# Performance work log

Measured on AMD Instinct MI355X. Metric: run time of the kernel, lower is better.

## Reference

```python
import jax, jax.numpy as jnp
import numpy as np

N_NODES = 50000
N_EDGES = 800000
D = 128
NEG_SLOPE = 0.01
LN_EPS = 1e-5


def gcn_conv(x, W, b, src, dst, n_nodes):
    # Linear transform: [N, D_in] @ [D_in, D_out]
    h = x @ W
    # Symmetric degree normalization (self-loops already included in src/dst)
    deg = jax.ops.segment_sum(jnp.ones_like(dst, dtype=h.dtype), dst, num_segments=n_nodes)
    dinv = jnp.where(deg > 0, jax.lax.rsqrt(deg), 0.0)
    coef = dinv[src] * dinv[dst]                      # [E]
    msg = h[src] * coef[:, None]                      # gather + scale, [E, D]
    out = jax.ops.segment_sum(msg, dst, num_segments=n_nodes)  # scatter-add
    return out + b


def layer_norm(x, gamma, beta):
    mu = jnp.mean(x, axis=-1, keepdims=True)
    var = jnp.mean(jnp.square(x - mu), axis=-1, keepdims=True)
    return (x - mu) * jax.lax.rsqrt(var + LN_EPS) * gamma + beta


def setup_inputs() -> dict:
    key = jax.random.key(0)
    ks = jax.random.split(key, 8)
    x = jax.random.normal(ks[0], (N_NODES, D), dtype=jnp.float32)
    edge_index = jax.random.randint(ks[1], (2, N_EDGES), 0, N_NODES, dtype=jnp.int64)
    s = 1.0 / np.sqrt(D)
    W1 = jax.random.uniform(ks[2], (D, D), jnp.float32, -s, s)
    b1 = jnp.zeros((D,), jnp.float32)
    W2 = jax.random.uniform(ks[3], (D, D), jnp.float32, -s, s)
    b2 = jnp.zeros((D,), jnp.float32)
    ln1_g = jnp.ones((D,), jnp.float32)
    ln1_b = jnp.zeros((D,), jnp.float32)
    ln2_g = jnp.ones((D,), jnp.float32)
    ln2_b = jnp.zeros((D,), jnp.float32)
    return {"x": x, "edge_index": edge_index, "W1": W1, "b1": b1,
            "ln1_g": ln1_g, "ln1_b": ln1_b, "W2": W2, "b2": b2,
            "ln2_g": ln2_g, "ln2_b": ln2_b}


def reference(x, edge_index, W1, b1, ln1_g, ln1_b, W2, b2, ln2_g, ln2_b):
    n = x.shape[0]
    # add self-loops (PyG GCNConv default)
    loops = jnp.arange(n, dtype=edge_index.dtype)
    src = jnp.concatenate([edge_index[0], loops])
    dst = jnp.concatenate([edge_index[1], loops])

    residual = x
    h = gcn_conv(x, W1, b1, src, dst, n)
    h = jax.nn.leaky_relu(h, NEG_SLOPE)
    h = layer_norm(h + residual, ln1_g, ln1_b)
    h = gcn_conv(h, W2, b2, src, dst, n)
    return jax.nn.leaky_relu(layer_norm(h + residual, ln2_g, ln2_b), NEG_SLOPE)
```

## Files before the change

### kernel.cpp

```cpp
#include <hip/hip_runtime.h>
#include <hip/hip_bf16.h>

#define NN 50000
#define NE 800000
#define D 128
#define NEG_SLOPE 0.01f
#define LN_EPS 1e-5f

#define NPB 256
#define NB 196
#define CAP 6144
#define ECH 8192
#define NCH ((NE + ECH - 1) / ECH)
#define NWPK 128

typedef __attribute__((ext_vector_type(8))) short bf16x8;
typedef __attribute__((ext_vector_type(4))) float f32x4;
typedef __attribute__((ext_vector_type(4))) int i32x4;

__device__ inline unsigned short f2bf(float f) {
    unsigned u = __float_as_uint(f);
    unsigned r = 0x7FFFu + ((u >> 16) & 1u);
    return (unsigned short)((u + r) >> 16);
}
__device__ inline void bf2x(unsigned u, float& lo, float& hi) {
    lo = __uint_as_float(u << 16);
    hi = __uint_as_float(u & 0xFFFF0000u);
}

__global__ __launch_bounds__(256) void fused_a(const int* __restrict__ src,
                                               const int* __restrict__ dst,
                                               int* __restrict__ bcursor,
                                               unsigned* __restrict__ bedge,
                                               const float* __restrict__ W1,
                                               const float* __restrict__ W2,
                                               unsigned short* __restrict__ WT1,
                                               unsigned short* __restrict__ WT2,
                                               unsigned short* __restrict__ hbf,
                                               unsigned short* __restrict__ hbf2) {
    __shared__ int hist[NB], lcur[NB], gbase[NB];
    int bid = blockIdx.x, t = threadIdx.x;
    if (bid < NCH) {
        int e0 = bid * ECH;
        int ecnt = min(ECH, NE - e0);
        if (t < NB) hist[t] = 0;
        __syncthreads();
        for (int k = t; k < ecnt; k += 256) atomicAdd(&hist[dst[e0 + k] >> 8], 1);
        __syncthreads();
        if (t < NB) {
            gbase[t] = atomicAdd(&bcursor[t], hist[t]);
            lcur[t] = 0;
        }
        __syncthreads();
        for (int k = t; k < ecnt; k += 256) {
            int s = src[e0 + k], d = dst[e0 + k];
            int b = d >> 8;
            int p = atomicAdd(&lcur[b], 1);
            bedge[(size_t)b * CAP + gbase[b] + p] = (unsigned)s | ((unsigned)(d & 255) << 16);
        }
    } else {
        int tid = (bid - NCH) * 256 + t;
        if (tid < 32) {
            uint4 z = make_uint4(0u, 0u, 0u, 0u);
            if (tid < 16) *(uint4*)&hbf[(size_t)NN * D + tid * 8] = z;
            else          *(uint4*)&hbf2[(size_t)NN * D + (tid - 16) * 8] = z;
        }
        const float* W = (tid < D * D) ? W1 : W2;
        unsigned short* WT = (tid < D * D) ? WT1 : WT2;
        int id = tid & (D * D - 1);
        int nn = id & 127, k = id >> 7;
        WT[nn * 128 + k] = f2bf(W[k * 128 + nn]);
    }
}

__global__ __launch_bounds__(256) void fused_b(const unsigned* __restrict__ bedge,
                                               const int* __restrict__ bcnt,
                                               float* __restrict__ dinv,
                                               int2* __restrict__ rowinfo,
                                               int* __restrict__ ticket,
                                               int* __restrict__ csr_src) {
    __shared__ int h[NPB];
    __shared__ int tmp[256];
    __shared__ int rl[NPB], cur[NPB];
    __shared__ int base;
    int b = blockIdx.x, t = threadIdx.x;
    h[t] = 0;
    __syncthreads();
    int s0 = b * CAP, s1 = s0 + bcnt[b];
    for (int k = s0 + t; k < s1; k += 256) atomicAdd(&h[bedge[k] >> 16], 1);
    __syncthreads();
    int deg = h[t];
    int node = b * NPB + t;
    int pdeg = (deg + 7) & ~7;
    tmp[t] = pdeg;
    __syncthreads();
    for (int off = 1; off < 256; off <<= 1) {
        int uu = (t >= off) ? tmp[t - off] : 0;
        __syncthreads();
        tmp[t] += uu;
        __syncthreads();
    }
    if (t == 255) base = atomicAdd(ticket, tmp[255]);
    __syncthreads();
    int start = base + tmp[t] - pdeg;
    rl[t] = start;
    cur[t] = 0;
    if (node < NN) {
        dinv[node] = rsqrtf((float)(deg + 1));
        rowinfo[node] = make_int2(start, pdeg);
    }
    __syncthreads();
    for (int k = s0 + t; k < s1; k += 256) {
        unsigned w = bedge[k];
        int li = w >> 16;
        int p = atomicAdd(&cur[li], 1);
        csr_src[rl[li] + p] = (int)(w & 0xFFFFu);
    }
    __syncthreads();
    int dgc = cur[t];
    int pend = (dgc + 7) & ~7;
    for (int k = dgc; k < pend; ++k)
        csr_src[rl[t] + k] = NN;
}

__global__ __launch_bounds__(256) void gemm_mfma(const float* __restrict__ A,
                                                 const unsigned short* __restrict__ WT,
                                                 const float* __restrict__ dinv,
                                                 unsigned short* __restrict__ out, int n) {
    __shared__ __align__(16) unsigned short a_lds[64 * 128];
    __shared__ __align__(16) unsigned short w_lds[128 * 128];
    int t = threadIdx.x;
    int m0 = blockIdx.x * 64;

    #pragma unroll
    for (int it = 0; it < 8; ++it) {
        int idx = it * 256 + t;
        int row = idx >> 4, c = idx & 15;
        uint4 v = *(const uint4*)&WT[row * 128 + c * 8];
        int byte = (row * 256 + c * 16) ^ ((row & 7) << 4);
        *(uint4*)((char*)w_lds + byte) = v;
    }
    #pragma unroll
    for (int it = 0; it < 4; ++it) {
        int idx = it * 256 + t;
        int row = idx >> 4, c = idx & 15;
        int grow = m0 + row;
        uint4 w = make_uint4(0u, 0u, 0u, 0u);
        if (grow < n) {
            float4 v0 = *(const float4*)&A[(size_t)grow * D + c * 8];
            float4 v1 = *(const float4*)&A[(size_t)grow * D + c * 8 + 4];
            w.x = (unsigned)f2bf(v0.x) | ((unsigned)f2bf(v0.y) << 16);
            w.y = (unsigned)f2bf(v0.z) | ((unsigned)f2bf(v0.w) << 16);
            w.z = (unsigned)f2bf(v1.x) | ((unsigned)f2bf(v1.y) << 16);
            w.w = (unsigned)f2bf(v1.z) | ((unsigned)f2bf(v1.w) << 16);
        }
        int byte = (row * 256 + c * 16) ^ ((row & 7) << 4);
        *(uint4*)((char*)a_lds + byte) = w;
    }
    __syncthreads();

    int wv = t >> 6, l = t & 63;
    int lrow = l & 15, lgrp = l >> 4;
    int arow = wv * 16 + lrow;

    f32x4 acc[8];
    #pragma unroll
    for (int nf = 0; nf < 8; ++nf) acc[nf] = (f32x4){0.f, 0.f, 0.f, 0.f};

    #pragma unroll
    for (int kk = 0; kk < 4; ++kk) {
        int abyte = (arow * 256 + kk * 64 + lgrp * 16) ^ ((arow & 7) << 4);
        bf16x8 afrag = *(bf16x8*)((char*)a_lds + abyte);
        #pragma unroll
        for (int nf = 0; nf < 8; ++nf) {
            int bcol = nf * 16 + lrow;
            int bbyte = (bcol * 256 + kk * 64 + lgrp * 16) ^ ((bcol & 7) << 4);
            bf16x8 bfrag = *(bf16x8*)((char*)w_lds + bbyte);
            acc[nf] = __builtin_amdgcn_mfma_f32_16x16x32_bf16(afrag, bfrag, acc[nf], 0, 0, 0);
        }
    }

    #pragma unroll
    for (int r = 0; r < 4; ++r) {
        int grow = m0 + wv * 16 + lgrp * 4 + r;
        if (grow < n) {
            float dv = dinv[grow];
            #pragma unroll
            for (int nf = 0; nf < 8; ++nf)
                out[(size_t)grow * D + nf * 16 + lrow] = f2bf(dv * acc[nf][r]);
        }
    }
}


__device__ inline void agg8s(const unsigned* __restrict__ h, const int* __restrict__ csr,
                             int e, int lane, float& ax_, float& ay_) {
    i32x4 s0 = __builtin_nontemporal_load((const i32x4*)(csr + e));
    i32x4 s1 = __builtin_nontemporal_load((const i32x4*)(csr + e + 4));
    unsigned g0 = h[(size_t)s0[0] * (D / 2) + lane];
    unsigned g1 = h[(size_t)s0[1] * (D / 2) + lane];
    unsigned g2 = h[(size_t)s0[2] * (D / 2) + lane];
    unsigned g3 = h[(size_t)s0[3] * (D / 2) + lane];
    unsigned g4 = h[(size_t)s1[0] * (D / 2) + lane];
    unsigned g5 = h[(size_t)s1[1] * (D / 2) + lane];
    unsigned g6 = h[(size_t)s1[2] * (D / 2) + lane];
    unsigned g7 = h[(size_t)s1[3] * (D / 2) + lane];
    float lo, hi;
    bf2x(g0, lo, hi); ax_ += lo; ay_ += hi;
    bf2x(g1, lo, hi); ax_ += lo; ay_ += hi;
    bf2x(g2, lo, hi); ax_ += lo; ay_ += hi;
    bf2x(g3, lo, hi); ax_ += lo; ay_ += hi;
    bf2x(g4, lo, hi); ax_ += lo; ay_ += hi;
    bf2x(g5, lo, hi); ax_ += lo; ay_ += hi;
    bf2x(g6, lo, hi); ax_ += lo; ay_ += hi;
    bf2x(g7, lo, hi); ax_ += lo; ay_ += hi;
}

__device__ inline void agg_2node(const unsigned* __restrict__ h,
                                 const int* __restrict__ csr,
                                 int eA, int eA1, int eB, int eB1, int lane,
                                 float& aAx, float& aAy, float& aBx, float& aBy) {
    while (eA + 16 <= eA1 && eB + 16 <= eB1) {
        i32x4 sA0 = __builtin_nontemporal_load((const i32x4*)(csr + eA));
        i32x4 sA1 = __builtin_nontemporal_load((const i32x4*)(csr + eA + 4));
        i32x4 sA2 = __builtin_nontemporal_load((const i32x4*)(csr + eA + 8));
        i32x4 sA3 = __builtin_nontemporal_load((const i32x4*)(csr + eA + 12));
        i32x4 sB0 = __builtin_nontemporal_load((const i32x4*)(csr + eB));
        i32x4 sB1 = __builtin_nontemporal_load((const i32x4*)(csr + eB + 4));
        i32x4 sB2 = __builtin_nontemporal_load((const i32x4*)(csr + eB + 8));
        i32x4 sB3 = __builtin_nontemporal_load((const i32x4*)(csr + eB + 12));
        unsigned gA0 = h[(size_t)sA0[0] * (D / 2) + lane];
        unsigned gA1 = h[(size_t)sA0[1] * (D / 2) + lane];
        unsigned gA2 = h[(size_t)sA0[2] * (D / 2) + lane];
        unsigned gA3 = h[(size_t)sA0[3] * (D / 2) + lane];
        unsigned gA4 = h[(size_t)sA1[0] * (D / 2) + lane];
        unsigned gA5 = h[(size_t)sA1[1] * (D / 2) + lane];
        unsigned gA6 = h[(size_t)sA1[2] * (D / 2) + lane];
        unsigned gA7 = h[(size_t)sA1[3] * (D / 2) + lane];
        unsigned gA8 = h[(size_t)sA2[0] * (D / 2) + lane];
        unsigned gA9 = h[(size_t)sA2[1] * (D / 2) + lane];
        unsigned gAa = h[(size_t)sA2[2] * (D / 2) + lane];
        unsigned gAb = h[(size_t)sA2[3] * (D / 2) + lane];
        unsigned gAc = h[(size_t)sA3[0] * (D / 2) + lane];
        unsigned gAd = h[(size_t)sA3[1] * (D / 2) + lane];
        unsigned gAe = h[(size_t)sA3[2] * (D / 2) + lane];
        unsigned gAf = h[(size_t)sA3[3] * (D / 2) + lane];
        unsigned gB0 = h[(size_t)sB0[0] * (D / 2) + lane];
        unsigned gB1 = h[(size_t)sB0[1] * (D / 2) + lane];
        unsigned gB2 = h[(size_t)sB0[2] * (D / 2) + lane];
        unsigned gB3 = h[(size_t)sB0[3] * (D / 2) + lane];
        unsigned gB4 = h[(size_t)sB1[0] * (D / 2) + lane];
        unsigned gB5 = h[(size_t)sB1[1] * (D / 2) + lane];
        unsigned gB6 = h[(size_t)sB1[2] * (D / 2) + lane];
        unsigned gB7 = h[(size_t)sB1[3] * (D / 2) + lane];
        unsigned gB8 = h[(size_t)sB2[0] * (D / 2) + lane];
        unsigned gB9 = h[(size_t)sB2[1] * (D / 2) + lane];
        unsigned gBa = h[(size_t)sB2[2] * (D / 2) + lane];
        unsigned gBb = h[(size_t)sB2[3] * (D / 2) + lane];
        unsigned gBc = h[(size_t)sB3[0] * (D / 2) + lane];
        unsigned gBd = h[(size_t)sB3[1] * (D / 2) + lane];
        unsigned gBe = h[(size_t)sB3[2] * (D / 2) + lane];
        unsigned gBf = h[(size_t)sB3[3] * (D / 2) + lane];
        float lo, hi;
        bf2x(gA0, lo, hi); aAx += lo; aAy += hi;
        bf2x(gA1, lo, hi); aAx += lo; aAy += hi;
        bf2x(gA2, lo, hi); aAx += lo; aAy += hi;
        bf2x(gA3, lo, hi); aAx += lo; aAy += hi;
        bf2x(gA4, lo, hi); aAx += lo; aAy += hi;
        bf2x(gA5, lo, hi); aAx += lo; aAy += hi;
        bf2x(gA6, lo, hi); aAx += lo; aAy += hi;
        bf2x(gA7, lo, hi); aAx += lo; aAy += hi;
        bf2x(gA8, lo, hi); aAx += lo; aAy += hi;
        bf2x(gA9, lo, hi); aAx += lo; aAy += hi;
        bf2x(gAa, lo, hi); aAx += lo; aAy += hi;
        bf2x(gAb, lo, hi); aAx += lo; aAy += hi;
        bf2x(gAc, lo, hi); aAx += lo; aAy += hi;
        bf2x(gAd, lo, hi); aAx += lo; aAy += hi;
        bf2x(gAe, lo, hi); aAx += lo; aAy += hi;
        bf2x(gAf, lo, hi); aAx += lo; aAy += hi;
        bf2x(gB0, lo, hi); aBx += lo; aBy += hi;
        bf2x(gB1, lo, hi); aBx += lo; aBy += hi;
        bf2x(gB2, lo, hi); aBx += lo; aBy += hi;
        bf2x(gB3, lo, hi); aBx += lo; aBy += hi;
        bf2x(gB4, lo, hi); aBx += lo; aBy += hi;
        bf2x(gB5, lo, hi); aBx += lo; aBy += hi;
        bf2x(gB6, lo, hi); aBx += lo; aBy += hi;
        bf2x(gB7, lo, hi); aBx += lo; aBy += hi;
        bf2x(gB8, lo, hi); aBx += lo; aBy += hi;
        bf2x(gB9, lo, hi); aBx += lo; aBy += hi;
        bf2x(gBa, lo, hi); aBx += lo; aBy += hi;
        bf2x(gBb, lo, hi); aBx += lo; aBy += hi;
        bf2x(gBc, lo, hi); aBx += lo; aBy += hi;
        bf2x(gBd, lo, hi); aBx += lo; aBy += hi;
        bf2x(gBe, lo, hi); aBx += lo; aBy += hi;
        bf2x(gBf, lo, hi); aBx += lo; aBy += hi;
        eA += 16; eB += 16;
    }
    while (eA + 8 <= eA1 && eB + 8 <= eB1) {
        agg8s(h, csr, eA, lane, aAx, aAy);
        agg8s(h, csr, eB, lane, aBx, aBy);
        eA += 8; eB += 8;
    }
    while (eA < eA1) { agg8s(h, csr, eA, lane, aAx, aAy); eA += 8; }
    while (eB < eB1) { agg8s(h, csr, eB, lane, aBx, aBy); eB += 8; }
}

__global__ __launch_bounds__(512) void agg_ln1_gemm(const unsigned* __restrict__ h,
                                                    const float* __restrict__ x,
                                                    const float* __restrict__ bias,
                                                    const float* __restrict__ gamma,
                                                    const float* __restrict__ beta,
                                                    const float* __restrict__ dinv,
                                                    const int2* __restrict__ rowinfo,
                                                    const int* __restrict__ csr_src,
                                                    const unsigned short* __restrict__ wt2,
                                                    unsigned short* __restrict__ hbf2) {
    __shared__ __align__(16) unsigned short w_lds[128 * 128];
    __shared__ __align__(16) unsigned short a_lds[16 * 128];
    int t = threadIdx.x;

    #pragma unroll
    for (int it = 0; it < 4; ++it) {
        int idx = it * 512 + t;
        int row = idx >> 4, c = idx & 15;
        uint4 v = *(const uint4*)&wt2[row * 128 + c * 8];
        int byte = (row * 256 + c * 16) ^ ((row & 7) << 4);
        *(uint4*)((char*)w_lds + byte) = v;
    }

    int wid = t >> 6, lane = t & 63;
    int iA = blockIdx.x * 16 + wid * 2;
    int iB = iA + 1;
    float diA = dinv[iA], diB = dinv[iB];

    float aAx, aAy, aBx, aBy;
    bf2x(h[(size_t)iA * (D / 2) + lane], aAx, aAy);
    bf2x(h[(size_t)iB * (D / 2) + lane], aBx, aBy);

    int2 riA = rowinfo[iA];
    int2 riB = rowinfo[iB];
    int eA = __builtin_amdgcn_readfirstlane(riA.x);
    int eA1 = eA + __builtin_amdgcn_readfirstlane(riA.y);
    int eB = __builtin_amdgcn_readfirstlane(riB.x);
    int eB1 = eB + __builtin_amdgcn_readfirstlane(riB.y);
    agg_2node(h, csr_src, eA, eA1, eB, eB1, lane, aAx, aAy, aBx, aBy);

    float2 bv = *(const float2*)&bias[2 * lane];
    float2 gv = *(const float2*)&gamma[2 * lane];
    float2 bt = *(const float2*)&beta[2 * lane];

    aAx = fmaf(diA, aAx, bv.x); aAy = fmaf(diA, aAy, bv.y);
    aBx = fmaf(diB, aBx, bv.x); aBy = fmaf(diB, aBy, bv.y);
    aAx = aAx > 0.f ? aAx : NEG_SLOPE * aAx;
    aAy = aAy > 0.f ? aAy : NEG_SLOPE * aAy;
    aBx = aBx > 0.f ? aBx : NEG_SLOPE * aBx;
    aBy = aBy > 0.f ? aBy : NEG_SLOPE * aBy;

    size_t rowA = (size_t)iA * D + 2 * lane;
    size_t rowB = (size_t)iB * D + 2 * lane;
    float2 xA = *(const float2*)&x[rowA];
    float2 xB = *(const float2*)&x[rowB];
    float vA0 = aAx + xA.x, vA1 = aAy + xA.y;
    float vB0 = aBx + xB.x, vB1 = aBy + xB.y;

    float sA1 = vA0 + vA1, sA2 = vA0 * vA0 + vA1 * vA1;
    float sB1 = vB0 + vB1, sB2 = vB0 * vB0 + vB1 * vB1;
    #pragma unroll
    for (int off = 1; off < 64; off <<= 1) {
        sA1 += __shfl_xor(sA1, off, 64);
        sA2 += __shfl_xor(sA2, off, 64);
        sB1 += __shfl_xor(sB1, off, 64);
        sB2 += __shfl_xor(sB2, off, 64);
    }
    float muA = sA1 * (1.f / 128.f);
    float varA = fmaxf(sA2 * (1.f / 128.f) - muA * muA, 0.f);
    float rsA = rsqrtf(varA + LN_EPS);
    float muB = sB1 * (1.f / 128.f);
    float varB = fmaxf(sB2 * (1.f / 128.f) - muB * muB, 0.f);
    float rsB = rsqrtf(varB + LN_EPS);

    float oA0 = (vA0 - muA) * rsA * gv.x + bt.x;
    float oA1 = (vA1 - muA) * rsA * gv.y + bt.y;
    float oB0 = (vB0 - muB) * rsB * gv.x + bt.x;
    float oB1 = (vB1 - muB) * rsB * gv.y + bt.y;

    int rA = wid * 2, rB = wid * 2 + 1;
    unsigned dwA = (unsigned)f2bf(oA0) | ((unsigned)f2bf(oA1) << 16);
    unsigned dwB = (unsigned)f2bf(oB0) | ((unsigned)f2bf(oB1) << 16);
    int byteA = (rA * 256 + lane * 4) ^ ((rA & 7) << 4);
    int byteB = (rB * 256 + lane * 4) ^ ((rB & 7) << 4);
    *(unsigned*)((char*)a_lds + byteA) = dwA;
    *(unsigned*)((char*)a_lds + byteB) = dwB;
    __syncthreads();

    int lrow = lane & 15, lgrp = lane >> 4;
    f32x4 acc = (f32x4){0.f, 0.f, 0.f, 0.f};
    #pragma unroll
    for (int kk = 0; kk < 4; ++kk) {
        int abyte = (lrow * 256 + kk * 64 + lgrp * 16) ^ ((lrow & 7) << 4);
        bf16x8 afrag = *(bf16x8*)((char*)a_lds + abyte);
        int bcol = wid * 16 + lrow;
        int bbyte = (bcol * 256 + kk * 64 + lgrp * 16) ^ ((bcol & 7) << 4);
        bf16x8 bfrag = *(bf16x8*)((char*)w_lds + bbyte);
        acc = __builtin_amdgcn_mfma_f32_16x16x32_bf16(afrag, bfrag, acc, 0, 0, 0);
    }
    #pragma unroll
    for (int r = 0; r < 4; ++r) {
        int grow = blockIdx.x * 16 + lgrp * 4 + r;
        hbf2[(size_t)grow * D + wid * 16 + lrow] = f2bf(dinv[grow] * acc[r]);
    }
}

__global__ __launch_bounds__(256) void agg_ln2(const unsigned* __restrict__ h,
                                               const float* __restrict__ x,
                                               const float* __restrict__ bias,
                                               const float* __restrict__ gamma,
                                               const float* __restrict__ beta,
                                               const float* __restrict__ dinv,
                                               const int2* __restrict__ rowinfo,
                                               const int* __restrict__ csr_src,
                                               float* __restrict__ out) {
    int wid = threadIdx.x >> 6;
    int lane = threadIdx.x & 63;
    int iA = blockIdx.x * 8 + wid * 2;
    int iB = iA + 1;
    float diA = dinv[iA], diB = dinv[iB];

    float aAx, aAy, aBx, aBy;
    bf2x(h[(size_t)iA * (D / 2) + lane], aAx, aAy);
    bf2x(h[(size_t)iB * (D / 2) + lane], aBx, aBy);

    int2 riA = rowinfo[iA];
    int2 riB = rowinfo[iB];
    int eA = __builtin_amdgcn_readfirstlane(riA.x);
    int eA1 = eA + __builtin_amdgcn_readfirstlane(riA.y);
    int eB = __builtin_amdgcn_readfirstlane(riB.x);
    int eB1 = eB + __builtin_amdgcn_readfirstlane(riB.y);
    agg_2node(h, csr_src, eA, eA1, eB, eB1, lane, aAx, aAy, aBx, aBy);

    float2 bv = *(const float2*)&bias[2 * lane];
    float2 gv = *(const float2*)&gamma[2 * lane];
    float2 bt = *(const float2*)&beta[2 * lane];

    aAx = fmaf(diA, aAx, bv.x); aAy = fmaf(diA, aAy, bv.y);
    aBx = fmaf(diB, aBx, bv.x); aBy = fmaf(diB, aBy, bv.y);
    size_t rowA = (size_t)iA * D + 2 * lane;
    size_t rowB = (size_t)iB * D + 2 * lane;
    float2 xA = *(const float2*)&x[rowA];
    float2 xB = *(const float2*)&x[rowB];
    float vA0 = aAx + xA.x, vA1 = aAy + xA.y;
    float vB0 = aBx + xB.x, vB1 = aBy + xB.y;

    float sA1 = vA0 + vA1, sA2 = vA0 * vA0 + vA1 * vA1;
    float sB1 = vB0 + vB1, sB2 = vB0 * vB0 + vB1 * vB1;
    #pragma unroll
    for (int off = 1; off < 64; off <<= 1) {
        sA1 += __shfl_xor(sA1, off, 64);
        sA2 += __shfl_xor(sA2, off, 64);
        sB1 += __shfl_xor(sB1, off, 64);
        sB2 += __shfl_xor(sB2, off, 64);
    }
    float muA = sA1 * (1.f / 128.f);
    float varA = fmaxf(sA2 * (1.f / 128.f) - muA * muA, 0.f);
    float rsA = rsqrtf(varA + LN_EPS);
    float muB = sB1 * (1.f / 128.f);
    float varB = fmaxf(sB2 * (1.f / 128.f) - muB * muB, 0.f);
    float rsB = rsqrtf(varB + LN_EPS);

    float oA0 = (vA0 - muA) * rsA * gv.x + bt.x;
    float oA1 = (vA1 - muA) * rsA * gv.y + bt.y;
    float oB0 = (vB0 - muB) * rsB * gv.x + bt.x;
    float oB1 = (vB1 - muB) * rsB * gv.y + bt.y;
    oA0 = oA0 > 0.f ? oA0 : NEG_SLOPE * oA0;
    oA1 = oA1 > 0.f ? oA1 : NEG_SLOPE * oA1;
    oB0 = oB0 > 0.f ? oB0 : NEG_SLOPE * oB0;
    oB1 = oB1 > 0.f ? oB1 : NEG_SLOPE * oB1;
    *(float2*)&out[rowA] = make_float2(oA0, oA1);
    *(float2*)&out[rowB] = make_float2(oB0, oB1);
}

extern "C" void kernel_launch(void* const* d_in, const int* in_sizes, int n_in,
                              void* d_out, int out_size, void* d_ws, size_t ws_size,
                              hipStream_t stream) {
    const float* x    = (const float*)d_in[0];
    const int*   ei   = (const int*)d_in[1];
    const float* W1   = (const float*)d_in[2];
    const float* b1   = (const float*)d_in[3];
    const float* ln1g = (const float*)d_in[4];
    const float* ln1b = (const float*)d_in[5];
    const float* W2   = (const float*)d_in[6];
    const float* b2   = (const float*)d_in[7];
    const float* ln2g = (const float*)d_in[8];
    const float* ln2b = (const float*)d_in[9];
    float* out = (float*)d_out;

    const int* srcp = ei;
    const int* dstp = ei + NE;

    char* ws = (char*)d_ws;
    size_t p = 0;
    auto alloc = [&](size_t bytes) {
        char* r = ws + p;
        p += (bytes + 255) & ~(size_t)255;
        return r;
    };
    int*      bcursor  = (int*)alloc((NB + 1) * 4);
    int2*     rowinfo  = (int2*)alloc((size_t)NN * 8);
    float*    dinv     = (float*)alloc(NN * 4);
    unsigned* bedge    = (unsigned*)alloc((size_t)NB * CAP * 4);
    int*      csr_src  = (int*)alloc(((size_t)NE + 8 * NN) * 4);
    unsigned short* hbf  = (unsigned short*)alloc((size_t)(NN + 8) * D * 2);
    unsigned short* hbf2 = (unsigned short*)alloc((size_t)(NN + 8) * D * 2);
    unsigned short* wt1  = (unsigned short*)alloc(D * D * 2);
    unsigned short* wt2  = (unsigned short*)alloc(D * D * 2);

    hipMemsetAsync(bcursor, 0, (NB + 1) * 4, stream);

    fused_a<<<NCH + NWPK, 256, 0, stream>>>(srcp, dstp, bcursor, bedge,
                                            W1, W2, wt1, wt2, hbf, hbf2);

    fused_b<<<NB, 256, 0, stream>>>(bedge, bcursor, dinv, rowinfo,
                                    &bcursor[NB], csr_src);

    gemm_mfma<<<(NN + 63) / 64, 256, 0, stream>>>(x, wt1, dinv, hbf, NN);

    agg_ln1_gemm<<<NN / 16, 512, 0, stream>>>((const unsigned*)hbf, x, b1, ln1g, ln1b,
                                              dinv, rowinfo, csr_src, wt2, hbf2);

    agg_ln2<<<NN / 8, 256, 0, stream>>>((const unsigned*)hbf2, x, b2, ln2g, ln2b,
                                        dinv, rowinfo, csr_src, out);
}
```

Baseline: 126.2 us.

## Compute degrees via global atomics and co-launch CSR fill with first GEMM

Degree counting moves into fused_a as extra blocks doing global atomic increments per edge. A tiny dinv_rowinfo kernel then builds dinv and row offsets. The CSR fill blocks and the first MFMA GEMM blocks are merged into one launch sharing LDS through a union, so the GEMM no longer waits behind the CSR construction. This trades a separate launch and serialization for 800k extra global atomics and one more small kernel.

```diff
diff --git a/kernel.cpp b/kernel.cpp
--- a/kernel.cpp
+++ b/kernel.cpp
@@ -12,7 +12,9 @@
 #define CAP 6144
 #define ECH 8192
 #define NCH ((NE + ECH - 1) / ECH)
+#define NDEG 256
 #define NWPK 128
+#define NGEMM ((NN + 63) / 64)
 
 typedef __attribute__((ext_vector_type(8))) short bf16x8;
 typedef __attribute__((ext_vector_type(4))) float f32x4;
@@ -32,6 +34,7 @@
                                                const int* __restrict__ dst,
                                                int* __restrict__ bcursor,
                                                unsigned* __restrict__ bedge,
+                                               int* __restrict__ deg,
                                                const float* __restrict__ W1,
                                                const float* __restrict__ W2,
                                                unsigned short* __restrict__ WT1,
@@ -58,8 +61,11 @@
             int p = atomicAdd(&lcur[b], 1);
             bedge[(size_t)b * CAP + gbase[b] + p] = (unsigned)s | ((unsigned)(d & 255) << 16);
         }
+    } else if (bid < NCH + NDEG) {
+        for (int k = (bid - NCH) * 256 + t; k < NE; k += NDEG * 256)
+            atomicAdd(&deg[dst[k]], 1);
     } else {
-        int tid = (bid - NCH) * 256 + t;
+        int tid = (bid - NCH - NDEG) * 256 + t;
         if (tid < 32) {
             uint4 z = make_uint4(0u, 0u, 0u, 0u);
             if (tid < 16) *(uint4*)&hbf[(size_t)NN * D + tid * 8] = z;
@@ -73,25 +79,16 @@
     }
 }
 
-__global__ __launch_bounds__(256) void fused_b(const unsigned* __restrict__ bedge,
-                                               const int* __restrict__ bcnt,
-                                               float* __restrict__ dinv,
-                                               int2* __restrict__ rowinfo,
-                                               int* __restrict__ ticket,
-                                               int* __restrict__ csr_src) {
-    __shared__ int h[NPB];
+__global__ __launch_bounds__(256) void dinv_rowinfo(const int* __restrict__ deg,
+                                                    float* __restrict__ dinv,
+                                                    int2* __restrict__ rowinfo,
+                                                    int* __restrict__ ticket) {
     __shared__ int tmp[256];
-    __shared__ int rl[NPB], cur[NPB];
     __shared__ int base;
     int b = blockIdx.x, t = threadIdx.x;
-    h[t] = 0;
-    __syncthreads();
-    int s0 = b * CAP, s1 = s0 + bcnt[b];
-    for (int k = s0 + t; k < s1; k += 256) atomicAdd(&h[bedge[k] >> 16], 1);
-    __syncthreads();
-    int deg = h[t];
     int node = b * NPB + t;
-    int pdeg = (deg + 7) & ~7;
+    int dg = (node < NN) ? deg[node] : 0;
+    int pdeg = (dg + 7) & ~7;
     tmp[t] = pdeg;
     __syncthreads();
     for (int off = 1; off < 256; off <<= 1) {
@@ -102,92 +99,111 @@
     }
     if (t == 255) base = atomicAdd(ticket, tmp[255]);
     __syncthreads();
-    int start = base + tmp[t] - pdeg;
-    rl[t] = start;
-    cur[t] = 0;
     if (node < NN) {
-        dinv[node] = rsqrtf((float)(deg + 1));
-        rowinfo[node] = make_int2(start, pdeg);
-    }
-    __syncthreads();
-    for (int k = s0 + t; k < s1; k += 256) {
-        unsigned w = bedge[k];
-        int li = w >> 16;
-        int p = atomicAdd(&cur[li], 1);
-        csr_src[rl[li] + p] = (int)(w & 0xFFFFu);
-    }
-    __syncthreads();
-    int dgc = cur[t];
-    int pend = (dgc + 7) & ~7;
-    for (int k = dgc; k < pend; ++k)
-        csr_src[rl[t] + k] = NN;
-}
-
-__global__ __launch_bounds__(256) void gemm_mfma(const float* __restrict__ A,
-                                                 const unsigned short* __restrict__ WT,
-                                                 const float* __restrict__ dinv,
-                                                 unsigned short* __restrict__ out, int n) {
-    __shared__ __align__(16) unsigned short a_lds[64 * 128];
-    __shared__ __align__(16) unsigned short w_lds[128 * 128];
-    int t = threadIdx.x;
-    int m0 = blockIdx.x * 64;
-
-    #pragma unroll
-    for (int it = 0; it < 8; ++it) {
-        int idx = it * 256 + t;
-        int row = idx >> 4, c = idx & 15;
-        uint4 v = *(const uint4*)&WT[row * 128 + c * 8];
-        int byte = (row * 256 + c * 16) ^ ((row & 7) << 4);
-        *(uint4*)((char*)w_lds + byte) = v;
-    }
-    #pragma unroll
-    for (int it = 0; it < 4; ++it) {
-        int idx = it * 256 + t;
-        int row = idx >> 4, c = idx & 15;
-        int grow = m0 + row;
-        uint4 w = make_uint4(0u, 0u, 0u, 0u);
-        if (grow < n) {
-            float4 v0 = *(const float4*)&A[(size_t)grow * D + c * 8];
-            float4 v1 = *(const float4*)&A[(size_t)grow * D + c * 8 + 4];
-            w.x = (unsigned)f2bf(v0.x) | ((unsigned)f2bf(v0.y) << 16);
-            w.y = (unsigned)f2bf(v0.z) | ((unsigned)f2bf(v0.w) << 16);
-            w.z = (unsigned)f2bf(v1.x) | ((unsigned)f2bf(v1.y) << 16);
-            w.w = (unsigned)f2bf(v1.z) | ((unsigned)f2bf(v1.w) << 16);
-        }
-        int byte = (row * 256 + c * 16) ^ ((row & 7) << 4);
-        *(uint4*)((char*)a_lds + byte) = w;
-    }
-    __syncthreads();
-
-    int wv = t >> 6, l = t & 63;
-    int lrow = l & 15, lgrp = l >> 4;
-    int arow = wv * 16 + lrow;
-
-    f32x4 acc[8];
-    #pragma unroll
-    for (int nf = 0; nf < 8; ++nf) acc[nf] = (f32x4){0.f, 0.f, 0.f, 0.f};
-
-    #pragma unroll
-    for (int kk = 0; kk < 4; ++kk) {
-        int abyte = (arow * 256 + kk * 64 + lgrp * 16) ^ ((arow & 7) << 4);
-        bf16x8 afrag = *(bf16x8*)((char*)a_lds + abyte);
+        dinv[node] = rsqrtf((float)(dg + 1));
+        rowinfo[node] = make_int2(base + tmp[t] - pdeg, pdeg);
+    }
+}
+
+struct CsrLDS { int rl[NPB], cur[NPB], pd[NPB]; };
+struct GemmLDS {
+    unsigned short a[64 * 128];
+    unsigned short w[128 * 128];
+};
+union BgLDS { CsrLDS c; GemmLDS g; };
+
+__global__ __launch_bounds__(256) void fused_bg(const unsigned* __restrict__ bedge,
+                                                const int* __restrict__ bcnt,
+                                                const int2* __restrict__ rowinfo,
+                                                int* __restrict__ csr_src,
+                                                const float* __restrict__ A,
+                                                const unsigned short* __restrict__ WT,
+                                                const float* __restrict__ dinv,
+                                                unsigned short* __restrict__ out) {
+    __shared__ BgLDS u;
+    int bid = blockIdx.x, t = threadIdx.x;
+
+    if (bid < NB) {
+        CsrLDS& L = u.c;
+        int b = bid;
+        int node = b * NPB + t;
+        int2 ri = (node < NN) ? rowinfo[node] : make_int2(0, 0);
+        L.rl[t] = ri.x;
+        L.pd[t] = ri.y;
+        L.cur[t] = 0;
+        __syncthreads();
+        int s0 = b * CAP, s1 = s0 + bcnt[b];
+        for (int k = s0 + t; k < s1; k += 256) {
+            unsigned w = bedge[k];
+            int li = w >> 16;
+            int p = atomicAdd(&L.cur[li], 1);
+            csr_src[L.rl[li] + p] = (int)(w & 0xFFFFu);
+        }
+        __syncthreads();
+        int dgc = L.cur[t];
+        int pend = L.pd[t];
+        for (int k = dgc; k < pend; ++k)
+            csr_src[L.rl[t] + k] = NN;
+    } else {
+        GemmLDS& L = u.g;
+        int m0 = (bid - NB) * 64;
         #pragma unroll
-        for (int nf = 0; nf < 8; ++nf) {
-            int bcol = nf * 16 + lrow;
-            int bbyte = (bcol * 256 + kk * 64 + lgrp * 16) ^ ((bcol & 7) << 4);
-            bf16x8 bfrag = *(bf16x8*)((char*)w_lds + bbyte);
-            acc[nf] = __builtin_amdgcn_mfma_f32_16x16x32_bf16(afrag, bfrag, acc[nf], 0, 0, 0);
-        }
-    }
-
-    #pragma unroll
-    for (int r = 0; r < 4; ++r) {
-        int grow = m0 + wv * 16 + lgrp * 4 + r;
-        if (grow < n) {
-            float dv = dinv[grow];
+        for (int it = 0; it < 8; ++it) {
+            int idx = it * 256 + t;
+            int row = idx >> 4, c = idx & 15;
+            uint4 v = *(const uint4*)&WT[row * 128 + c * 8];
+            int byte = (row * 256 + c * 16) ^ ((row & 7) << 4);
+            *(uint4*)((char*)L.w + byte) = v;
+        }
+        #pragma unroll
+        for (int it = 0; it < 4; ++it) {
+            int idx = it * 256 + t;
+            int row = idx >> 4, c = idx & 15;
+            int grow = m0 + row;
+            uint4 w = make_uint4(0u, 0u, 0u, 0u);
+            if (grow < NN) {
+                float4 v0 = *(const float4*)&A[(size_t)grow * D + c * 8];
+                float4 v1 = *(const float4*)&A[(size_t)grow * D + c * 8 + 4];
+                w.x = (unsigned)f2bf(v0.x) | ((unsigned)f2bf(v0.y) << 16);
+                w.y = (unsigned)f2bf(v0.z) | ((unsigned)f2bf(v0.w) << 16);
+                w.z = (unsigned)f2bf(v1.x) | ((unsigned)f2bf(v1.y) << 16);
+                w.w = (unsigned)f2bf(v1.z) | ((unsigned)f2bf(v1.w) << 16);
+            }
+            int byte = (row * 256 + c * 16) ^ ((row & 7) << 4);
+            *(uint4*)((char*)L.a + byte) = w;
+        }
+        __syncthreads();
+
+        int wv = t >> 6, l = t & 63;
+        int lrow = l & 15, lgrp = l >> 4;
+        int arow = wv * 16 + lrow;
+
+        f32x4 acc[8];
+        #pragma unroll
+        for (int nf = 0; nf < 8; ++nf) acc[nf] = (f32x4){0.f, 0.f, 0.f, 0.f};
+
+        #pragma unroll
+        for (int kk = 0; kk < 4; ++kk) {
+            int abyte = (arow * 256 + kk * 64 + lgrp * 16) ^ ((arow & 7) << 4);
+            bf16x8 afrag = *(bf16x8*)((char*)L.a + abyte);
             #pragma unroll
-            for (int nf = 0; nf < 8; ++nf)
-                out[(size_t)grow * D + nf * 16 + lrow] = f2bf(dv * acc[nf][r]);
+            for (int nf = 0; nf < 8; ++nf) {
+                int bcol = nf * 16 + lrow;
+                int bbyte = (bcol * 256 + kk * 64 + lgrp * 16) ^ ((bcol & 7) << 4);
+                bf16x8 bfrag = *(bf16x8*)((char*)L.w + bbyte);
+                acc[nf] = __builtin_amdgcn_mfma_f32_16x16x32_bf16(afrag, bfrag, acc[nf], 0, 0, 0);
+            }
+        }
+
+        #pragma unroll
+        for (int r = 0; r < 4; ++r) {
+            int grow = m0 + wv * 16 + lgrp * 4 + r;
+            if (grow < NN) {
+                float dv = dinv[grow];
+                #pragma unroll
+                for (int nf = 0; nf < 8; ++nf)
+                    out[(size_t)grow * D + nf * 16 + lrow] = f2bf(dv * acc[nf][r]);
+            }
         }
     }
 }
@@ -504,6 +520,7 @@
         p += (bytes + 255) & ~(size_t)255;
         return r;
     };
+    int*      deg      = (int*)alloc(NN * 4);
     int*      bcursor  = (int*)alloc((NB + 1) * 4);
     int2*     rowinfo  = (int2*)alloc((size_t)NN * 8);
     float*    dinv     = (float*)alloc(NN * 4);
@@ -514,15 +531,16 @@
     unsigned short* wt1  = (unsigned short*)alloc(D * D * 2);
     unsigned short* wt2  = (unsigned short*)alloc(D * D * 2);
 
-    hipMemsetAsync(bcursor, 0, (NB + 1) * 4, stream);
-
-    fused_a<<<NCH + NWPK, 256, 0, stream>>>(srcp, dstp, bcursor, bedge,
-                                            W1, W2, wt1, wt2, hbf, hbf2);
-
-    fused_b<<<NB, 256, 0, stream>>>(bedge, bcursor, dinv, rowinfo,
-                                    &bcursor[NB], csr_src);
-
-    gemm_mfma<<<(NN + 63) / 64, 256, 0, stream>>>(x, wt1, dinv, hbf, NN);
+    size_t zbytes = (char*)rowinfo - (char*)deg;
+    hipMemsetAsync(deg, 0, zbytes, stream);
+
+    fused_a<<<NCH + NDEG + NWPK, 256, 0, stream>>>(srcp, dstp, bcursor, bedge, deg,
+                                                   W1, W2, wt1, wt2, hbf, hbf2);
+
+    dinv_rowinfo<<<NB, 256, 0, stream>>>(deg, dinv, rowinfo, &bcursor[NB]);
+
+    fused_bg<<<NB + NGEMM, 256, 0, stream>>>(bedge, bcursor, rowinfo, csr_src,
+                                             x, wt1, dinv, hbf);
 
     agg_ln1_gemm<<<NN / 16, 512, 0, stream>>>((const unsigned*)hbf, x, b1, ln1g, ln1b,
                                               dinv, rowinfo, csr_src, wt2, hbf2);
```

Measured after the change: 148.3 us. 1.18x slower.
